# Performance work log

Measured on AMD Instinct MI355X. Metric: run time of the kernel, lower is better.

Reference implementation:

```python
import jax, jax.numpy as jnp
import numpy as np

N_NODES = 50000
N_EDGES = 800000
D_IN = 512
D_OUT = 256


def setup_inputs() -> dict:
    key = jax.random.key(0)
    k1, k2, k3 = jax.random.split(key, 3)
    x = jax.random.normal(k1, (N_NODES, D_IN), dtype=jnp.float32)
    edge_index = jax.random.randint(k2, (2, N_EDGES), 0, N_NODES, dtype=jnp.int64)
    # Glorot-style init for the GCN weight, zero bias (PyG defaults)
    W = jax.random.normal(k3, (D_IN, D_OUT), dtype=jnp.float32) * (1.0 / np.sqrt(D_IN))
    b = jnp.zeros((D_OUT,), dtype=jnp.float32)
    return {"x": x, "edge_index": edge_index, "W": W, "b": b}


def reference(x, edge_index, W, b):
    N = x.shape[0]
    # 1) dense linear transform (the compute-heavy GEMM)
    xw = x @ W  # [N, d_out]

    # 2) add self-loops (PyG GCNConv default)
    loop = jnp.arange(N, dtype=edge_index.dtype)
    row = jnp.concatenate([edge_index[0], loop])  # sources
    col = jnp.concatenate([edge_index[1], loop])  # targets

    # 3) symmetric normalization deg^{-1/2} on targets (in-degree incl. self-loops)
    deg = jax.ops.segment_sum(jnp.ones_like(col, dtype=xw.dtype), col, num_segments=N)
    dinv = jnp.where(deg > 0, jax.lax.rsqrt(deg), 0.0)
    norm = dinv[row] * dinv[col]  # [E+N]

    # 4) gather source features, scale, scatter-add to targets
    msgs = xw[row] * norm[:, None]  # [E+N, d_out]
    agg = jax.ops.segment_sum(msgs, col, num_segments=N)  # [N, d_out]

    # 5) bias + ReLU (dropout is identity in eval mode)
    return jax.nn.relu(agg + b)
```

## Files before the change

### kernel.cpp

```cpp
#include <hip/hip_runtime.h>
#include <hip/hip_bf16.h>

#define N_NODES 50000
#define N_EDGES 800000
#define D_IN    512
#define D_OUT   256
#define NBLK_SCAN ((N_NODES + 1023) / 1024)
#define GEMM_NWG (((N_NODES + 127) / 128) * 2)
#define GEMM_Q   (GEMM_NWG / 8)
#define GEMM_R   (GEMM_NWG % 8)

typedef short s8v  __attribute__((ext_vector_type(8)));
typedef float f32x4 __attribute__((ext_vector_type(4)));

__device__ __forceinline__ unsigned short bf16b(float f) {
    __hip_bfloat16 h = __float2bfloat16(f);
    return *reinterpret_cast<unsigned short*>(&h);
}

#define GLD16(gp, lp)                                                           \
    __builtin_amdgcn_global_load_lds(                                           \
        (const __attribute__((address_space(1))) unsigned int*)(const void*)(gp),\
        (__attribute__((address_space(3))) unsigned int*)(void*)(lp), 16, 0, 0)

__device__ __forceinline__ int wave_incl_scan(int v, int lane) {
    #pragma unroll
    for (int d = 1; d < 64; d <<= 1) {
        int u = __shfl_up(v, d, 64);
        if (lane >= d) v += u;
    }
    return v;
}


__global__ void k_count(const int* __restrict__ col, int* __restrict__ cnt) {
    int i = blockIdx.x * 256 + threadIdx.x;
    if (i < N_EDGES) atomicAdd(&cnt[col[i]], 1);
}

__launch_bounds__(256)
__global__ void k_scan1(const int* __restrict__ cnt, int* __restrict__ bsum) {
    const int t = threadIdx.x, b = blockIdx.x;
    const int idx = b * 1024 + t * 4;
    int4 v = make_int4(0, 0, 0, 0);
    if (idx < N_NODES) v = *(const int4*)&cnt[idx];
    int s = v.x + v.y + v.z + v.w;
    #pragma unroll
    for (int d = 1; d < 64; d <<= 1) s += __shfl_xor(s, d, 64);
    __shared__ int ws[4];
    if ((t & 63) == 0) ws[t >> 6] = s;
    __syncthreads();
    if (t == 0) bsum[b] = ws[0] + ws[1] + ws[2] + ws[3];
}

__global__ void k_scan2(const int* __restrict__ bsum, int* __restrict__ boff) {
    const int t = threadIdx.x;
    int v = (t < NBLK_SCAN) ? bsum[t] : 0;
    int inc = wave_incl_scan(v, t);
    if (t < NBLK_SCAN) boff[t] = inc - v;
}

__launch_bounds__(256)
__global__ void k_scan3(const int* __restrict__ cnt, const int* __restrict__ boff,
                        int* __restrict__ row_ptr, float* __restrict__ dinv,
                        int* __restrict__ cursor) {
    const int t = threadIdx.x, b = blockIdx.x;
    const int lane = t & 63, wv = t >> 6;
    const int idx = b * 1024 + t * 4;
    int4 v = make_int4(0, 0, 0, 0);
    if (idx < N_NODES) v = *(const int4*)&cnt[idx];
    int s = v.x + v.y + v.z + v.w;
    int isc = wave_incl_scan(s, lane);
    __shared__ int wsum[4];
    if (lane == 63) wsum[wv] = isc;
    __syncthreads();
    int off = boff[b];
    #pragma unroll
    for (int i = 0; i < 4; ++i)
        if (i < wv) off += wsum[i];
    int p0 = off + isc - s;
    int p1 = p0 + v.x;
    int p2 = p1 + v.y;
    int p3 = p2 + v.z;
    if (idx < N_NODES) {
        row_ptr[idx + 0] = p0; cursor[idx + 0] = p0; dinv[idx + 0] = rsqrtf(1.f + (float)v.x);
        row_ptr[idx + 1] = p1; cursor[idx + 1] = p1; dinv[idx + 1] = rsqrtf(1.f + (float)v.y);
        row_ptr[idx + 2] = p2; cursor[idx + 2] = p2; dinv[idx + 2] = rsqrtf(1.f + (float)v.z);
        row_ptr[idx + 3] = p3; cursor[idx + 3] = p3; dinv[idx + 3] = rsqrtf(1.f + (float)v.w);
    }
    if (b == 0 && t == 0) row_ptr[N_NODES] = N_EDGES;
}

__global__ void k_fill(const int* __restrict__ row, const int* __restrict__ col,
                       int* __restrict__ cursor, int* __restrict__ csr_src) {
    int i = blockIdx.x * 256 + threadIdx.x;
    if (i < N_EDGES) {
        int pos = atomicAdd(&cursor[col[i]], 1);
        csr_src[pos] = row[i];
    }
}

__global__ void k_wt(const float* __restrict__ W, unsigned short* __restrict__ Wt) {
    int k = blockIdx.x;
    int n = threadIdx.x;
    Wt[(size_t)n * D_IN + k] = bf16b(W[(size_t)k * D_OUT + n]);
}

__launch_bounds__(256)
__global__ void k_xb(const float* __restrict__ x, const float* __restrict__ dinv,
                     unsigned short* __restrict__ xb) {
    int idx = blockIdx.x * 256 + threadIdx.x;
    const int tot = N_NODES * D_IN / 8;
    if (idx >= tot) return;
    int node = idx >> 6;
    float s = dinv[node];
    const float4* src = (const float4*)x + (size_t)idx * 2;
    float4 v0 = src[0], v1 = src[1];
    union { uint4 q; unsigned short h[8]; } pk;
    pk.h[0] = bf16b(v0.x * s); pk.h[1] = bf16b(v0.y * s);
    pk.h[2] = bf16b(v0.z * s); pk.h[3] = bf16b(v0.w * s);
    pk.h[4] = bf16b(v1.x * s); pk.h[5] = bf16b(v1.y * s);
    pk.h[6] = bf16b(v1.z * s); pk.h[7] = bf16b(v1.w * s);
    ((uint4*)xb)[idx] = pk.q;
}

__launch_bounds__(256)
__global__ void k_gemm(const unsigned short* __restrict__ xb,
                       const unsigned short* __restrict__ Wt,
                       unsigned short* __restrict__ yb)
{
    __shared__ __align__(16) unsigned short As[128 * 64];
    __shared__ __align__(16) unsigned short Bs[128 * 64];

    int orig = blockIdx.x;
    int xcd = orig % 8, pos = orig / 8;
    int wg = (xcd < GEMM_R) ? xcd * (GEMM_Q + 1) + pos
                            : GEMM_R * (GEMM_Q + 1) + (xcd - GEMM_R) * GEMM_Q + pos;
    const int nt = wg & 1;
    const int mt = wg >> 1;
    const int m0 = mt * 128;
    const int n0 = nt * 128;

    const int t  = threadIdx.x;
    const int w  = t >> 6;
    const int l  = t & 63;
    const int wm = (w >> 1) * 64;
    const int wn = (w & 1) * 64;
    const int lr = l & 15;
    const int lk = l >> 4;
    const int aswz = (lr & 7) << 4;

    const int srow = l >> 3;
    const int srcj = (l & 7) ^ srow;

    size_t aoff[4];
    size_t boff[4];
    #pragma unroll
    for (int i = 0; i < 4; ++i) {
        int g = w * 4 + i;
        int am = m0 + g * 8 + srow;
        if (am >= N_NODES) am = 0;
        aoff[i] = (size_t)am * D_IN + srcj * 8;
        int bn = n0 + g * 8 + srow;
        boff[i] = (size_t)bn * D_IN + srcj * 8;
    }

    f32x4 acc[4][4] = {};

    for (int kk = 0; kk < D_IN; kk += 64) {
        #pragma unroll
        for (int i = 0; i < 4; ++i) {
            int g = w * 4 + i;
            GLD16(&xb[aoff[i] + kk], (char*)As + g * 1024);
            GLD16(&Wt[boff[i] + kk], (char*)Bs + g * 1024);
        }
        __syncthreads();

        #pragma unroll
        for (int ks = 0; ks < 2; ++ks) {
            const int kb = (ks * 64 + lk * 16) ^ aswz;
            s8v af[4], bfr[4];
            #pragma unroll
            for (int f = 0; f < 4; ++f)
                af[f]  = *(const s8v*)((const char*)As + ((wm + f * 16 + lr) * 128 + kb));
            #pragma unroll
            for (int f = 0; f < 4; ++f)
                bfr[f] = *(const s8v*)((const char*)Bs + ((wn + f * 16 + lr) * 128 + kb));
            #pragma unroll
            for (int fm = 0; fm < 4; ++fm)
                #pragma unroll
                for (int fn = 0; fn < 4; ++fn)
                    acc[fm][fn] = __builtin_amdgcn_mfma_f32_16x16x32_bf16(
                        af[fm], bfr[fn], acc[fm][fn], 0, 0, 0);
        }
        __syncthreads();
    }

    #pragma unroll
    for (int fm = 0; fm < 4; ++fm) {
        #pragma unroll
        for (int j = 0; j < 4; ++j) {
            int row = m0 + wm + fm * 16 + lk * 4 + j;
            if (row < N_NODES) {
                #pragma unroll
                for (int fn = 0; fn < 4; ++fn) {
                    int col = n0 + wn + fn * 16 + lr;
                    yb[(size_t)row * D_OUT + col] = bf16b(acc[fm][fn][j]);
                }
            }
        }
    }
}

__device__ __forceinline__ void add8(float* acc, uint4 q) {
    unsigned x;
    x = q.x; acc[0] += __uint_as_float(x << 16); acc[1] += __uint_as_float(x & 0xffff0000u);
    x = q.y; acc[2] += __uint_as_float(x << 16); acc[3] += __uint_as_float(x & 0xffff0000u);
    x = q.z; acc[4] += __uint_as_float(x << 16); acc[5] += __uint_as_float(x & 0xffff0000u);
    x = q.w; acc[6] += __uint_as_float(x << 16); acc[7] += __uint_as_float(x & 0xffff0000u);
}

__launch_bounds__(256)
__global__ void k_gather(const int* __restrict__ row_ptr, const int* __restrict__ csr_src,
                         const unsigned short* __restrict__ yb, const float* __restrict__ dinv,
                         const float* __restrict__ bias, float* __restrict__ out)
{
    const int c  = blockIdx.x * 4 + (threadIdx.x >> 6);
    const int l  = threadIdx.x & 63;
    const int eg = l >> 5;
    const int cs = l & 31;
    const size_t colb = (size_t)cs * 8;

    float acc[8] = {0.f,0.f,0.f,0.f,0.f,0.f,0.f,0.f};

    const int s = row_ptr[c];
    const int e = row_ptr[c + 1];

    int i = s + eg;
    while (i + 14 < e) {
        int r[8];
        #pragma unroll
        for (int u = 0; u < 8; ++u) r[u] = csr_src[i + 2 * u];
        uint4 v[8];
        #pragma unroll
        for (int u = 0; u < 8; ++u) v[u] = *(const uint4*)&yb[(size_t)r[u] * D_OUT + colb];
        #pragma unroll
        for (int u = 0; u < 8; ++u) add8(acc, v[u]);
        i += 16;
    }
    if (i + 6 < e) {
        int r[4];
        #pragma unroll
        for (int u = 0; u < 4; ++u) r[u] = csr_src[i + 2 * u];
        uint4 v[4];
        #pragma unroll
        for (int u = 0; u < 4; ++u) v[u] = *(const uint4*)&yb[(size_t)r[u] * D_OUT + colb];
        #pragma unroll
        for (int u = 0; u < 4; ++u) add8(acc, v[u]);
        i += 8;
    }
    while (i < e) {
        int r = csr_src[i];
        uint4 v = *(const uint4*)&yb[(size_t)r * D_OUT + colb];
        add8(acc, v);
        i += 2;
    }

    #pragma unroll
    for (int u = 0; u < 8; ++u) acc[u] += __shfl_xor(acc[u], 32, 64);

    uint4 sv = *(const uint4*)&yb[(size_t)c * D_OUT + colb];
    add8(acc, sv);

    if (eg == 0) {
        const float sc = dinv[c];
        float4 b0 = *(const float4*)&bias[colb];
        float4 b1 = *(const float4*)&bias[colb + 4];
        float4 o0, o1;
        o0.x = fmaxf(fmaf(acc[0], sc, b0.x), 0.f);
        o0.y = fmaxf(fmaf(acc[1], sc, b0.y), 0.f);
        o0.z = fmaxf(fmaf(acc[2], sc, b0.z), 0.f);
        o0.w = fmaxf(fmaf(acc[3], sc, b0.w), 0.f);
        o1.x = fmaxf(fmaf(acc[4], sc, b1.x), 0.f);
        o1.y = fmaxf(fmaf(acc[5], sc, b1.y), 0.f);
        o1.z = fmaxf(fmaf(acc[6], sc, b1.z), 0.f);
        o1.w = fmaxf(fmaf(acc[7], sc, b1.w), 0.f);
        float* dst = &out[(size_t)c * D_OUT + colb];
        *(float4*)dst       = o0;
        *(float4*)(dst + 4) = o1;
    }
}

extern "C" void kernel_launch(void* const* d_in, const int* in_sizes, int n_in,
                              void* d_out, int out_size, void* d_ws, size_t ws_size,
                              hipStream_t stream) {
    const float* x   = (const float*)d_in[0];
    const int*   ei  = (const int*)d_in[1];
    const float* W   = (const float*)d_in[2];
    const float* b   = (const float*)d_in[3];
    float*       out = (float*)d_out;

    const int* row = ei;
    const int* col = ei + N_EDGES;

    char* p = (char*)d_ws;
    unsigned short* yb = (unsigned short*)p;  p += (size_t)N_NODES * D_OUT * 2;
    unsigned short* xb = (unsigned short*)p;  p += (size_t)N_NODES * D_IN * 2;
    unsigned short* Wt = (unsigned short*)p;  p += (size_t)D_OUT * D_IN * 2;
    int*   csr_src = (int*)p;                 p += (size_t)N_EDGES * 4;
    int*   cnt     = (int*)p;                 p += (size_t)N_NODES * 4;
    int*   row_ptr = (int*)p;                 p += (size_t)(N_NODES + 4) * 4;
    int*   cursor  = (int*)p;                 p += (size_t)N_NODES * 4;
    float* dinv    = (float*)p;               p += (size_t)N_NODES * 4;
    int*   bsum    = (int*)p;                 p += (size_t)NBLK_SCAN * 4;
    int*   boff    = (int*)p;                 p += (size_t)NBLK_SCAN * 4;

    hipMemsetAsync(cnt, 0, (size_t)N_NODES * sizeof(int), stream);
    k_count<<<(N_EDGES + 255) / 256, 256, 0, stream>>>(col, cnt);
    k_scan1<<<NBLK_SCAN, 256, 0, stream>>>(cnt, bsum);
    k_scan2<<<1, 64, 0, stream>>>(bsum, boff);
    k_scan3<<<NBLK_SCAN, 256, 0, stream>>>(cnt, boff, row_ptr, dinv, cursor);
    k_fill <<<(N_EDGES + 255) / 256, 256, 0, stream>>>(row, col, cursor, csr_src);
    k_wt   <<<D_IN, D_OUT, 0, stream>>>(W, Wt);
    k_xb   <<<(N_NODES * D_IN / 8 + 255) / 256, 256, 0, stream>>>(x, dinv, xb);

    k_gemm<<<GEMM_NWG, 256, 0, stream>>>(xb, Wt, yb);

    k_gather<<<N_NODES / 4, 256, 0, stream>>>(row_ptr, csr_src, yb, dinv, b, out);
}
```

Measured before the change: 213.6 us.

## Fuse fp32-to-bf16 conversion into GEMM and simplify gather to one wave per node

Removes the separate pre-pass that scaled x by dinv and converted it to a bf16 buffer. The GEMM now loads fp32 x straight into LDS, converts to bf16 while building MFMA fragments, and applies the dinv row scale in the epilogue. This drops a full write and re-read of the bf16 copy of x, but the GEMM now moves twice as many A bytes and spends more LDS and ALU work on conversion. The gather kernel is also rewritten: each wave handles one node with lane-wide uint2 loads and a predicated 16-edge unrolled loop, instead of two half-wave edge groups combined by a shuffle.

Measured after the change: 234.5 us. +9.8%, slower.

```diff
diff --git a/kernel.cpp b/kernel.cpp
--- a/kernel.cpp
+++ b/kernel.cpp
@@ -17,6 +17,8 @@
     __hip_bfloat16 h = __float2bfloat16(f);
     return *reinterpret_cast<unsigned short*>(&h);
 }
+__device__ __forceinline__ float bflo(unsigned u) { return __uint_as_float(u << 16); }
+__device__ __forceinline__ float bfhi(unsigned u) { return __uint_as_float(u & 0xffff0000u); }
 
 #define GLD16(gp, lp)                                                           \
     __builtin_amdgcn_global_load_lds(                                           \
@@ -107,29 +109,12 @@
 }
 
 __launch_bounds__(256)
-__global__ void k_xb(const float* __restrict__ x, const float* __restrict__ dinv,
-                     unsigned short* __restrict__ xb) {
-    int idx = blockIdx.x * 256 + threadIdx.x;
-    const int tot = N_NODES * D_IN / 8;
-    if (idx >= tot) return;
-    int node = idx >> 6;
-    float s = dinv[node];
-    const float4* src = (const float4*)x + (size_t)idx * 2;
-    float4 v0 = src[0], v1 = src[1];
-    union { uint4 q; unsigned short h[8]; } pk;
-    pk.h[0] = bf16b(v0.x * s); pk.h[1] = bf16b(v0.y * s);
-    pk.h[2] = bf16b(v0.z * s); pk.h[3] = bf16b(v0.w * s);
-    pk.h[4] = bf16b(v1.x * s); pk.h[5] = bf16b(v1.y * s);
-    pk.h[6] = bf16b(v1.z * s); pk.h[7] = bf16b(v1.w * s);
-    ((uint4*)xb)[idx] = pk.q;
-}
-
-__launch_bounds__(256)
-__global__ void k_gemm(const unsigned short* __restrict__ xb,
+__global__ void k_gemm(const float* __restrict__ A,
                        const unsigned short* __restrict__ Wt,
+                       const float* __restrict__ dinv,
                        unsigned short* __restrict__ yb)
 {
-    __shared__ __align__(16) unsigned short As[128 * 64];
+    __shared__ __align__(16) float          As[128 * 64];
     __shared__ __align__(16) unsigned short Bs[128 * 64];
 
     int orig = blockIdx.x;
@@ -148,19 +133,23 @@
     const int wn = (w & 1) * 64;
     const int lr = l & 15;
     const int lk = l >> 4;
-    const int aswz = (lr & 7) << 4;
-
+
+    const int arow_l = l >> 4;
+    const int c32    = (l & 15) >> 1;
+    size_t aoff[8];
+    #pragma unroll
+    for (int i = 0; i < 8; ++i) {
+        int row = m0 + w * 32 + i * 4 + arow_l;
+        if (row >= N_NODES) row = 0;
+        int sc32 = c32 ^ (row & 7);
+        aoff[i] = (size_t)row * D_IN + sc32 * 8 + (l & 1) * 4;
+    }
     const int srow = l >> 3;
     const int srcj = (l & 7) ^ srow;
-
-    size_t aoff[4];
     size_t boff[4];
     #pragma unroll
     for (int i = 0; i < 4; ++i) {
         int g = w * 4 + i;
-        int am = m0 + g * 8 + srow;
-        if (am >= N_NODES) am = 0;
-        aoff[i] = (size_t)am * D_IN + srcj * 8;
         int bn = n0 + g * 8 + srow;
         boff[i] = (size_t)bn * D_IN + srcj * 8;
     }
@@ -169,20 +158,31 @@
 
     for (int kk = 0; kk < D_IN; kk += 64) {
         #pragma unroll
-        for (int i = 0; i < 4; ++i) {
-            int g = w * 4 + i;
-            GLD16(&xb[aoff[i] + kk], (char*)As + g * 1024);
-            GLD16(&Wt[boff[i] + kk], (char*)Bs + g * 1024);
-        }
+        for (int i = 0; i < 8; ++i)
+            GLD16(&A[aoff[i] + kk], (char*)As + (w * 32 + i * 4) * 256);
+        #pragma unroll
+        for (int i = 0; i < 4; ++i)
+            GLD16(&Wt[boff[i] + kk], (char*)Bs + (w * 4 + i) * 1024);
         __syncthreads();
 
         #pragma unroll
         for (int ks = 0; ks < 2; ++ks) {
-            const int kb = (ks * 64 + lk * 16) ^ aswz;
             s8v af[4], bfr[4];
             #pragma unroll
-            for (int f = 0; f < 4; ++f)
-                af[f]  = *(const s8v*)((const char*)As + ((wm + f * 16 + lr) * 128 + kb));
+            for (int f = 0; f < 4; ++f) {
+                int row = wm + f * 16 + lr;
+                int ch  = (ks * 4 + lk) ^ (lr & 7);
+                const char* p = (const char*)As + row * 256 + ch * 32;
+                float4 x0 = *(const float4*)p;
+                float4 x1 = *(const float4*)(p + 16);
+                union { s8v v; unsigned short h[8]; } u;
+                u.h[0] = bf16b(x0.x); u.h[1] = bf16b(x0.y);
+                u.h[2] = bf16b(x0.z); u.h[3] = bf16b(x0.w);
+                u.h[4] = bf16b(x1.x); u.h[5] = bf16b(x1.y);
+                u.h[6] = bf16b(x1.z); u.h[7] = bf16b(x1.w);
+                af[f] = u.v;
+            }
+            const int kb = (ks * 64 + lk * 16) ^ ((lr & 7) << 4);
             #pragma unroll
             for (int f = 0; f < 4; ++f)
                 bfr[f] = *(const s8v*)((const char*)Bs + ((wn + f * 16 + lr) * 128 + kb));
@@ -202,22 +202,15 @@
         for (int j = 0; j < 4; ++j) {
             int row = m0 + wm + fm * 16 + lk * 4 + j;
             if (row < N_NODES) {
+                float s = dinv[row];
                 #pragma unroll
                 for (int fn = 0; fn < 4; ++fn) {
                     int col = n0 + wn + fn * 16 + lr;
-                    yb[(size_t)row * D_OUT + col] = bf16b(acc[fm][fn][j]);
+                    yb[(size_t)row * D_OUT + col] = bf16b(acc[fm][fn][j] * s);
                 }
             }
         }
     }
-}
-
-__device__ __forceinline__ void add8(float* acc, uint4 q) {
-    unsigned x;
-    x = q.x; acc[0] += __uint_as_float(x << 16); acc[1] += __uint_as_float(x & 0xffff0000u);
-    x = q.y; acc[2] += __uint_as_float(x << 16); acc[3] += __uint_as_float(x & 0xffff0000u);
-    x = q.z; acc[4] += __uint_as_float(x << 16); acc[5] += __uint_as_float(x & 0xffff0000u);
-    x = q.w; acc[6] += __uint_as_float(x << 16); acc[7] += __uint_as_float(x & 0xffff0000u);
 }
 
 __launch_bounds__(256)
@@ -225,70 +218,45 @@
                          const unsigned short* __restrict__ yb, const float* __restrict__ dinv,
                          const float* __restrict__ bias, float* __restrict__ out)
 {
-    const int c  = blockIdx.x * 4 + (threadIdx.x >> 6);
-    const int l  = threadIdx.x & 63;
-    const int eg = l >> 5;
-    const int cs = l & 31;
-    const size_t colb = (size_t)cs * 8;
-
-    float acc[8] = {0.f,0.f,0.f,0.f,0.f,0.f,0.f,0.f};
+    const int c = blockIdx.x * 4 + (threadIdx.x >> 6);
+    const int l = threadIdx.x & 63;
+    const uint2* y2 = (const uint2*)yb;
+
+    uint2 sv = y2[(size_t)c * 64 + l];
+    float acc0 = bflo(sv.x), acc1 = bfhi(sv.x);
+    float acc2 = bflo(sv.y), acc3 = bfhi(sv.y);
 
     const int s = row_ptr[c];
     const int e = row_ptr[c + 1];
 
-    int i = s + eg;
-    while (i + 14 < e) {
-        int r[8];
-        #pragma unroll
-        for (int u = 0; u < 8; ++u) r[u] = csr_src[i + 2 * u];
-        uint4 v[8];
-        #pragma unroll
-        for (int u = 0; u < 8; ++u) v[u] = *(const uint4*)&yb[(size_t)r[u] * D_OUT + colb];
-        #pragma unroll
-        for (int u = 0; u < 8; ++u) add8(acc, v[u]);
-        i += 16;
-    }
-    if (i + 6 < e) {
-        int r[4];
-        #pragma unroll
-        for (int u = 0; u < 4; ++u) r[u] = csr_src[i + 2 * u];
-        uint4 v[4];
-        #pragma unroll
-        for (int u = 0; u < 4; ++u) v[u] = *(const uint4*)&yb[(size_t)r[u] * D_OUT + colb];
-        #pragma unroll
-        for (int u = 0; u < 4; ++u) add8(acc, v[u]);
-        i += 8;
-    }
-    while (i < e) {
-        int r = csr_src[i];
-        uint4 v = *(const uint4*)&yb[(size_t)r * D_OUT + colb];
-        add8(acc, v);
-        i += 2;
-    }
-
-    #pragma unroll
-    for (int u = 0; u < 8; ++u) acc[u] += __shfl_xor(acc[u], 32, 64);
-
-    uint4 sv = *(const uint4*)&yb[(size_t)c * D_OUT + colb];
-    add8(acc, sv);
-
-    if (eg == 0) {
-        const float sc = dinv[c];
-        float4 b0 = *(const float4*)&bias[colb];
-        float4 b1 = *(const float4*)&bias[colb + 4];
-        float4 o0, o1;
-        o0.x = fmaxf(fmaf(acc[0], sc, b0.x), 0.f);
-        o0.y = fmaxf(fmaf(acc[1], sc, b0.y), 0.f);
-        o0.z = fmaxf(fmaf(acc[2], sc, b0.z), 0.f);
-        o0.w = fmaxf(fmaf(acc[3], sc, b0.w), 0.f);
-        o1.x = fmaxf(fmaf(acc[4], sc, b1.x), 0.f);
-        o1.y = fmaxf(fmaf(acc[5], sc, b1.y), 0.f);
-        o1.z = fmaxf(fmaf(acc[6], sc, b1.z), 0.f);
-        o1.w = fmaxf(fmaf(acc[7], sc, b1.w), 0.f);
-        float* dst = &out[(size_t)c * D_OUT + colb];
-        *(float4*)dst       = o0;
-        *(float4*)(dst + 4) = o1;
-    }
+    for (int i = s; i < e; i += 16) {
+        int idx[16];
+        #pragma unroll
+        for (int j = 0; j < 16; ++j) {
+            int p = i + j;
+            idx[j] = csr_src[p < e ? p : e - 1];
+        }
+        uint2 v[16];
+        #pragma unroll
+        for (int j = 0; j < 16; ++j)
+            v[j] = y2[(size_t)idx[j] * 64 + l];
+        #pragma unroll
+        for (int j = 0; j < 16; ++j) {
+            if (i + j < e) {
+                acc0 += bflo(v[j].x); acc1 += bfhi(v[j].x);
+                acc2 += bflo(v[j].y); acc3 += bfhi(v[j].y);
+            }
+        }
+    }
+
+    const float sc = dinv[c];
+    float4 bb = ((const float4*)bias)[l];
+    float4 o;
+    o.x = fmaxf(fmaf(acc0, sc, bb.x), 0.f);
+    o.y = fmaxf(fmaf(acc1, sc, bb.y), 0.f);
+    o.z = fmaxf(fmaf(acc2, sc, bb.z), 0.f);
+    o.w = fmaxf(fmaf(acc3, sc, bb.w), 0.f);
+    ((float4*)out)[(size_t)c * 64 + l] = o;
 }
 
 extern "C" void kernel_launch(void* const* d_in, const int* in_sizes, int n_in,
@@ -305,7 +273,6 @@
 
     char* p = (char*)d_ws;
     unsigned short* yb = (unsigned short*)p;  p += (size_t)N_NODES * D_OUT * 2;
-    unsigned short* xb = (unsigned short*)p;  p += (size_t)N_NODES * D_IN * 2;
     unsigned short* Wt = (unsigned short*)p;  p += (size_t)D_OUT * D_IN * 2;
     int*   csr_src = (int*)p;                 p += (size_t)N_EDGES * 4;
     int*   cnt     = (int*)p;                 p += (size_t)N_NODES * 4;
@@ -322,9 +289,8 @@
     k_scan3<<<NBLK_SCAN, 256, 0, stream>>>(cnt, boff, row_ptr, dinv, cursor);
     k_fill <<<(N_EDGES + 255) / 256, 256, 0, stream>>>(row, col, cursor, csr_src);
     k_wt   <<<D_IN, D_OUT, 0, stream>>>(W, Wt);
-    k_xb   <<<(N_NODES * D_IN / 8 + 255) / 256, 256, 0, stream>>>(x, dinv, xb);
-
-    k_gemm<<<GEMM_NWG, 256, 0, stream>>>(xb, Wt, yb);
+
+    k_gemm<<<GEMM_NWG, 256, 0, stream>>>(x, Wt, dinv, yb);
 
     k_gather<<<N_NODES / 4, 256, 0, stream>>>(row_ptr, csr_src, yb, dinv, b, out);
 }
```
